# Performance work log

Hardware: AMD Instinct MI355X
Metric: run time of the kernel (lower is better)

## Reference

```python
import jax, jax.numpy as jnp
import numpy as np

N_NODES = 50000
N_EDGES = 800000
H_DIM = 128
N_REL = 40
N_BASES = 4


def setup_inputs() -> dict:
    key = jax.random.key(0)
    ks = jax.random.split(key, 9)
    h = jax.random.normal(ks[0], (N_NODES, H_DIM), jnp.float32)
    norm = jax.random.uniform(ks[1], (N_EDGES, 1), jnp.float32)
    basis_w = jax.random.normal(ks[2], (N_BASES, H_DIM, H_DIM), jnp.float32) * 0.05
    w_comp = jax.random.normal(ks[3], (N_REL, N_BASES), jnp.float32) * 0.5
    loop_w = jax.random.normal(ks[4], (H_DIM, H_DIM), jnp.float32) * 0.05
    bias = jax.random.normal(ks[5], (H_DIM,), jnp.float32) * 0.05
    src = jax.random.randint(ks[6], (N_EDGES,), 0, N_NODES, jnp.int32)
    dst = jax.random.randint(ks[7], (N_EDGES,), 0, N_NODES, jnp.int32)
    etype = jax.random.randint(ks[8], (N_EDGES,), 0, N_REL, jnp.int32)
    return {"h": h, "norm": norm, "basis_w": basis_w, "w_comp": w_comp,
            "loop_w": loop_w, "bias": bias, "src": src, "dst": dst, "etype": etype}


def reference(h, norm, basis_w, w_comp, loop_w, bias, src, dst, etype):
    # RelGraphConv with 'basis' regularizer, one layer (num_hidden_layers=1):
    #   W_r = sum_b w_comp[r, b] * basis_w[b]
    #   m_e = (h[src_e] @ W_{etype_e}) * norm_e
    #   agg[v] = sum_{e: dst_e = v} m_e
    #   out = relu(agg + bias + h @ loop_w)   (dropout = 0)
    # Contraction reordered for memory efficiency: scatter-add per-basis
    # scaled source features first (node-level), then apply small basis GEMMs.
    n = h.shape[0]
    n_bases = basis_w.shape[0]
    coeff = w_comp[etype] * norm          # [E, B] per-edge basis coefficients * norm
    h_src = h[src]                        # [E, D] edge-gathered source features
    agg = jnp.zeros((n, basis_w.shape[2]), dtype=h.dtype)
    for b in range(n_bases):              # small fixed loop over bases
        s_b = jax.ops.segment_sum(coeff[:, b:b + 1] * h_src, dst, num_segments=n)  # [N, D]
        agg = agg + s_b @ basis_w[b]
    return jax.nn.relu(agg + bias + h @ loop_w)
```

## Files before the change

### kernel.cpp

```cpp
#include <hip/hip_runtime.h>
#include <stdint.h>

#define N_NODES 50000
#define N_EDGES 800000
#define H_DIM 128
#define N_REL 40
#define N_BASES 4
#define N_RANGES 196
#define EP_BLOCKS 200
#define EDGES_PER_BLK 4000
#define STAGE_CAP 5120

typedef __attribute__((ext_vector_type(8))) short bf16x8;
typedef __attribute__((ext_vector_type(4))) float f32x4;

__device__ __forceinline__ unsigned short f2bf(float f) {
    unsigned int u = __float_as_uint(f);
    unsigned int r = u + 0x7fffu + ((u >> 16) & 1u);
    return (unsigned short)(r >> 16);
}

__global__ __launch_bounds__(256) void prep_kernel(
        const float* __restrict__ h,
        const float* __restrict__ basis_w, const float* __restrict__ loop_w,
        const int* __restrict__ src, const int* __restrict__ dst,
        const int* __restrict__ etype, const float* __restrict__ norm,
        unsigned short* __restrict__ A, unsigned short* __restrict__ wt3,
        uint2* __restrict__ pkd, int* __restrict__ gcnt) {
    int bid = blockIdx.x;
    if (bid < 3125) {
        int t = bid * 256 + threadIdx.x;
        int row = t >> 4;
        int cb = (t & 15) * 8;
        const float* p = h + (size_t)row * 128 + cb;
        float4 a0 = ((const float4*)p)[0];
        float4 a1 = ((const float4*)p)[1];
        bf16x8 o;
        o[0] = (short)f2bf(a0.x); o[1] = (short)f2bf(a0.y);
        o[2] = (short)f2bf(a0.z); o[3] = (short)f2bf(a0.w);
        o[4] = (short)f2bf(a1.x); o[5] = (short)f2bf(a1.y);
        o[6] = (short)f2bf(a1.z); o[7] = (short)f2bf(a1.w);
        *(bf16x8*)(A + (size_t)row * H_DIM + cb) = o;
    } else if (bid < 3130) {
        int mat = bid - 3125;
        const float* srcm = (mat < 4) ? (basis_w + mat * 16384) : loop_w;
        int koff = (mat < 4) ? (128 + mat * 128) : 0;
        int t = threadIdx.x;
#pragma unroll
        for (int i = 0; i < 16; ++i) {
            int f = t + i * 256;
            int k = f >> 5;
            int j4 = (f & 31) * 4;
            float4 v = ((const float4*)srcm)[f];
            int kg = koff + k;
            int ks = kg >> 5;
            int quad = (kg >> 3) & 3;
            int jj = kg & 7;
            float vv[4] = {v.x, v.y, v.z, v.w};
#pragma unroll
            for (int d = 0; d < 4; ++d) {
                int j = j4 + d;
                int cg = j >> 4;
                int n16 = j & 15;
                wt3[(size_t)((ks * 8 + cg) * 64 + quad * 16 + n16) * 8 + jj] =
                    f2bf(vv[d]);
            }
        }
    } else {
        __shared__ int lhist[N_RANGES];
        int blk = bid - 3130;
        int t = threadIdx.x;
        if (t < N_RANGES) lhist[t] = 0;
        __syncthreads();
        int e0 = blk * EDGES_PER_BLK;
        for (int i = t; i < EDGES_PER_BLK; i += 256) {
            int e = e0 + i;
            int d = dst[e];
            unsigned int nbf = f2bf(norm[e]);
            pkd[e] = make_uint2((unsigned)src[e] | ((unsigned)etype[e] << 20),
                                (unsigned)d | (nbf << 17));
            atomicAdd(&lhist[d >> 8], 1);
        }
        __syncthreads();
        if (t < N_RANGES) gcnt[t * EP_BLOCKS + blk] = lhist[t];
    }
}

__global__ __launch_bounds__(256) void bucket_scan_a(
        const int* __restrict__ gcnt, int* __restrict__ blkbase,
        int* __restrict__ btot) {
    __shared__ int wsum[4];
    int r = blockIdx.x;
    int t = threadIdx.x, lane = t & 63, w = t >> 6;
    int x = (t < EP_BLOCKS) ? gcnt[r * EP_BLOCKS + t] : 0;
    int v = x;
#pragma unroll
    for (int d = 1; d < 64; d <<= 1) {
        int y = __shfl_up(v, d);
        if (lane >= d) v += y;
    }
    if (lane == 63) wsum[w] = v;
    __syncthreads();
    int wpre = 0;
    if (w > 0) wpre += wsum[0];
    if (w > 1) wpre += wsum[1];
    if (w > 2) wpre += wsum[2];
    if (t < EP_BLOCKS) blkbase[r * EP_BLOCKS + t] = wpre + v - x;
    if (t == 255) btot[r] = wpre + v;
}

__global__ __launch_bounds__(256) void binscatter(
        const uint2* __restrict__ pkd, const int* __restrict__ blkbase,
        const int* __restrict__ btot, uint2* __restrict__ bucketed) {
    __shared__ int lcur[N_RANGES];
    __shared__ int wsum[4];
    int t = threadIdx.x, lane = t & 63, w = t >> 6;
    int x = (t < N_RANGES) ? btot[t] : 0;
    int v = x;
#pragma unroll
    for (int d = 1; d < 64; d <<= 1) {
        int y = __shfl_up(v, d);
        if (lane >= d) v += y;
    }
    if (lane == 63) wsum[w] = v;
    __syncthreads();
    int wpre = 0;
    if (w > 0) wpre += wsum[0];
    if (w > 1) wpre += wsum[1];
    if (w > 2) wpre += wsum[2];
    if (t < N_RANGES)
        lcur[t] = (wpre + v - x) + blkbase[t * EP_BLOCKS + blockIdx.x];
    __syncthreads();
    int e0 = blockIdx.x * EDGES_PER_BLK;
    for (int i = t; i < EDGES_PER_BLK; i += 256) {
        uint2 p = pkd[e0 + i];
        int r = (p.y & 0x1FFFF) >> 8;
        int pos = atomicAdd(&lcur[r], 1);
        bucketed[pos] = p;
    }
}

__global__ __launch_bounds__(256) void bucket_sort(
        const int* __restrict__ btot, const uint2* __restrict__ bucketed,
        uint2* __restrict__ sorted_pe, int* __restrict__ offs) {
    __shared__ int hist[256];
    __shared__ int cur[256];
    __shared__ int wsum[4];
    __shared__ int sbeg;
    __shared__ uint2 stage[STAGE_CAP];
    int r = blockIdx.x;
    int t = threadIdx.x, lane = t & 63, w = t >> 6;
    int x = (t < N_RANGES) ? btot[t] : 0;
    int v = x;
#pragma unroll
    for (int d = 1; d < 64; d <<= 1) {
        int y = __shfl_up(v, d);
        if (lane >= d) v += y;
    }
    if (lane == 63) wsum[w] = v;
    hist[t] = 0;
    __syncthreads();
    int wpre = 0;
    if (w > 0) wpre += wsum[0];
    if (w > 1) wpre += wsum[1];
    if (w > 2) wpre += wsum[2];
    if (t == r) sbeg = wpre + v - x;
    __syncthreads();
    int begin = sbeg;
    int end = begin + btot[r];
    int n = end - begin;
    for (int i = begin + t; i < end; i += 256)
        atomicAdd(&hist[bucketed[i].y & 255], 1);
    __syncthreads();
    int x2 = hist[t];
    int v2 = x2;
#pragma unroll
    for (int d = 1; d < 64; d <<= 1) {
        int y = __shfl_up(v2, d);
        if (lane >= d) v2 += y;
    }
    if (lane == 63) wsum[w] = v2;
    __syncthreads();
    int wpre2 = 0;
    if (w > 0) wpre2 += wsum[0];
    if (w > 1) wpre2 += wsum[1];
    if (w > 2) wpre2 += wsum[2];
    int excl_rel = wpre2 + v2 - x2;
    int node = r * 256 + t;
    if (node < N_NODES) offs[node] = begin + excl_rel;
    if (r == N_RANGES - 1 && t == 0) offs[N_NODES] = N_EDGES;
    cur[t] = excl_rel;
    __syncthreads();
    if (n <= STAGE_CAP) {
        for (int i = begin + t; i < end; i += 256) {
            uint2 p = bucketed[i];
            int pos = atomicAdd(&cur[p.y & 255], 1);
            stage[pos] = make_uint2(p.x, (p.y >> 17) << 16);
        }
        __syncthreads();
        for (int i = t; i < n; i += 256)
            sorted_pe[begin + i] = stage[i];
    } else {
        for (int i = begin + t; i < end; i += 256) {
            uint2 p = bucketed[i];
            int pos = atomicAdd(&cur[p.y & 255], 1);
            sorted_pe[begin + pos] = make_uint2(p.x, (p.y >> 17) << 16);
        }
    }
}

__global__ __launch_bounds__(256) void agg_gemm(
        const int* __restrict__ offs, const uint2* __restrict__ sorted_pe,
        const float* __restrict__ w_comp,
        const unsigned short* __restrict__ Ab,
        const unsigned short* __restrict__ wt3,
        const float* __restrict__ bias, float* __restrict__ out) {
    __shared__ __align__(16) unsigned short S[32 * 640];
    int wv = threadIdx.x >> 6;
    int lane = threadIdx.x & 63;
    int nbase = blockIdx.x * 32;
    const unsigned int* Au = (const unsigned int*)Ab;

    for (int q = 0; q < 8; ++q) {
        int row = (wv << 3) + q;
        int v = __builtin_amdgcn_readfirstlane(nbase + row);
        float a0l = 0.f, a0h = 0.f, a1l = 0.f, a1h = 0.f;
        float a2l = 0.f, a2h = 0.f, a3l = 0.f, a3h = 0.f;
        unsigned int hb = 0u;
        if (v < N_NODES) {
            hb = Au[(size_t)v * 64 + lane];
            int begin = offs[v];
            int end = offs[v + 1];
            int j = begin;
            for (; j + 8 <= end; j += 8) {
                uint2 p[8];
                unsigned int u[8];
#pragma unroll
                for (int k = 0; k < 8; ++k) p[k] = sorted_pe[j + k];
#pragma unroll
                for (int k = 0; k < 8; ++k)
                    u[k] = Au[(size_t)(p[k].x & 0xFFFFF) * 64 + lane];
#pragma unroll
                for (int k = 0; k < 8; ++k) {
                    float4 wc = ((const float4*)w_comp)[p[k].x >> 20];
                    float nm = __uint_as_float(p[k].y);
                    float lo = __uint_as_float(u[k] << 16);
                    float hi = __uint_as_float(u[k] & 0xffff0000u);
                    a0l += (wc.x * nm) * lo; a0h += (wc.x * nm) * hi;
                    a1l += (wc.y * nm) * lo; a1h += (wc.y * nm) * hi;
                    a2l += (wc.z * nm) * lo; a2h += (wc.z * nm) * hi;
                    a3l += (wc.w * nm) * lo; a3h += (wc.w * nm) * hi;
                }
            }
            for (; j < end; ++j) {
                uint2 p = sorted_pe[j];
                float4 wc = ((const float4*)w_comp)[p.x >> 20];
                float nm = __uint_as_float(p.y);
                unsigned int u = Au[(size_t)(p.x & 0xFFFFF) * 64 + lane];
                float lo = __uint_as_float(u << 16);
                float hi = __uint_as_float(u & 0xffff0000u);
                a0l += (wc.x * nm) * lo; a0h += (wc.x * nm) * hi;
                a1l += (wc.y * nm) * lo; a1h += (wc.y * nm) * hi;
                a2l += (wc.z * nm) * lo; a2h += (wc.z * nm) * hi;
                a3l += (wc.w * nm) * lo; a3h += (wc.w * nm) * hi;
            }
        }
        char* rp = (char*)S + row * 1280;
        int swz = (row & 7) << 4;
        *(unsigned int*)(rp + ((lane * 4) ^ swz)) = hb;
        *(unsigned int*)(rp + ((256 + lane * 4) ^ swz)) =
            (unsigned int)f2bf(a0l) | ((unsigned int)f2bf(a0h) << 16);
        *(unsigned int*)(rp + ((512 + lane * 4) ^ swz)) =
            (unsigned int)f2bf(a1l) | ((unsigned int)f2bf(a1h) << 16);
        *(unsigned int*)(rp + ((768 + lane * 4) ^ swz)) =
            (unsigned int)f2bf(a2l) | ((unsigned int)f2bf(a2h) << 16);
        *(unsigned int*)(rp + ((1024 + lane * 4) ^ swz)) =
            (unsigned int)f2bf(a3l) | ((unsigned int)f2bf(a3h) << 16);
    }
    __syncthreads();

    int n16 = lane & 15;
    int quad = lane >> 4;
    f32x4 acc[2][2];
#pragma unroll
    for (int rt = 0; rt < 2; ++rt)
#pragma unroll
        for (int c = 0; c < 2; ++c) acc[rt][c] = (f32x4)0.f;

    const char* a0p = (const char*)S + n16 * 1280;
    const char* a1p = (const char*)S + (16 + n16) * 1280;
    int swz2 = (n16 & 7) << 4;
    const unsigned short* bp = wt3 + (size_t)(wv * 2) * 512 + lane * 8;

#pragma unroll
    for (int ks = 0; ks < 20; ++ks) {
        int off = (ks * 64 + quad * 16) ^ swz2;
        bf16x8 a0 = *(const bf16x8*)(a0p + off);
        bf16x8 a1 = *(const bf16x8*)(a1p + off);
        bf16x8 b0 = *(const bf16x8*)(bp + (size_t)ks * 4096);
        bf16x8 b1 = *(const bf16x8*)(bp + (size_t)ks * 4096 + 512);
        acc[0][0] = __builtin_amdgcn_mfma_f32_16x16x32_bf16(a0, b0, acc[0][0], 0, 0, 0);
        acc[1][0] = __builtin_amdgcn_mfma_f32_16x16x32_bf16(a1, b0, acc[1][0], 0, 0, 0);
        acc[0][1] = __builtin_amdgcn_mfma_f32_16x16x32_bf16(a0, b1, acc[0][1], 0, 0, 0);
        acc[1][1] = __builtin_amdgcn_mfma_f32_16x16x32_bf16(a1, b1, acc[1][1], 0, 0, 0);
    }

#pragma unroll
    for (int rt = 0; rt < 2; ++rt) {
#pragma unroll
        for (int c = 0; c < 2; ++c) {
            int col = (wv * 2 + c) * 16 + n16;
            float bv = bias[col];
#pragma unroll
            for (int rg = 0; rg < 4; ++rg) {
                int r = nbase + rt * 16 + quad * 4 + rg;
                if (r < N_NODES)
                    out[(size_t)r * H_DIM + col] = fmaxf(acc[rt][c][rg] + bv, 0.f);
            }
        }
    }
}

extern "C" void kernel_launch(void* const* d_in, const int* in_sizes, int n_in,
                              void* d_out, int out_size, void* d_ws, size_t ws_size,
                              hipStream_t stream) {
    const float* h       = (const float*)d_in[0];
    const float* norm    = (const float*)d_in[1];
    const float* basis_w = (const float*)d_in[2];
    const float* w_comp  = (const float*)d_in[3];
    const float* loop_w  = (const float*)d_in[4];
    const float* bias    = (const float*)d_in[5];
    const int*   src     = (const int*)d_in[6];
    const int*   dst     = (const int*)d_in[7];
    const int*   etype   = (const int*)d_in[8];
    float* out = (float*)d_out;

    char* base = (char*)d_ws;
    unsigned short* wt3       = (unsigned short*)(base + 0);
    unsigned short* A         = (unsigned short*)(base + 163840);
    int*            offs      = (int*)(base + 12963840);
    uint2*          pkd       = (uint2*)(base + 13163848);
    uint2*          bucketed  = (uint2*)(base + 19563848);
    uint2*          sorted_pe = (uint2*)(base + 25963848);
    int*            gcnt      = (int*)(base + 32363848);
    int*            blkbase   = (int*)(base + 32520648);
    int*            btot      = (int*)(base + 32677448);

    prep_kernel<<<3330, 256, 0, stream>>>(h, basis_w, loop_w,
                                          src, dst, etype, norm,
                                          A, wt3, pkd, gcnt);
    bucket_scan_a<<<N_RANGES, 256, 0, stream>>>(gcnt, blkbase, btot);
    binscatter<<<EP_BLOCKS, 256, 0, stream>>>(pkd, blkbase, btot, bucketed);
    bucket_sort<<<N_RANGES, 256, 0, stream>>>(btot, bucketed, sorted_pe, offs);
    agg_gemm<<<1563, 256, 0, stream>>>(offs, sorted_pe, w_comp, A, wt3, bias, out);
}
```

Measured before the change: 193.3 us.

## Precompute per-edge basis coefficients in sort, split agg_gemm over 8 waves

The bucket sort now writes a separate source-index array and a float4 of w_comp[etype]*norm per edge, so the aggregation loop no longer gathers w_comp or multiplies by norm per edge. The aggregation kernel moves to 512 threads (8 waves, 4 rows each, one 16-column MFMA tile per wave). It also replaces the scalar tail loop with a masked 8-wide loop reading padded zero entries. The cost is more sorted-edge traffic (20 bytes per edge instead of 8), traded for less per-edge ALU work and more parallelism per block.

```diff
diff --git a/kernel.cpp b/kernel.cpp
--- a/kernel.cpp
+++ b/kernel.cpp
@@ -88,10 +88,15 @@
 
 __global__ __launch_bounds__(256) void bucket_scan_a(
         const int* __restrict__ gcnt, int* __restrict__ blkbase,
-        int* __restrict__ btot) {
+        int* __restrict__ btot, unsigned* __restrict__ sorted_src,
+        float4* __restrict__ sorted_cf) {
     __shared__ int wsum[4];
     int r = blockIdx.x;
     int t = threadIdx.x, lane = t & 63, w = t >> 6;
+    if (r == 0 && t < 16) {
+        sorted_src[N_EDGES + t] = 0u;
+        sorted_cf[N_EDGES + t] = make_float4(0.f, 0.f, 0.f, 0.f);
+    }
     int x = (t < EP_BLOCKS) ? gcnt[r * EP_BLOCKS + t] : 0;
     int v = x;
 #pragma unroll
@@ -142,7 +147,9 @@
 
 __global__ __launch_bounds__(256) void bucket_sort(
         const int* __restrict__ btot, const uint2* __restrict__ bucketed,
-        uint2* __restrict__ sorted_pe, int* __restrict__ offs) {
+        const float* __restrict__ w_comp,
+        unsigned* __restrict__ sorted_src, float4* __restrict__ sorted_cf,
+        int* __restrict__ offs) {
     __shared__ int hist[256];
     __shared__ int cur[256];
     __shared__ int wsum[4];
@@ -198,20 +205,30 @@
             stage[pos] = make_uint2(p.x, (p.y >> 17) << 16);
         }
         __syncthreads();
-        for (int i = t; i < n; i += 256)
-            sorted_pe[begin + i] = stage[i];
+        for (int i = t; i < n; i += 256) {
+            uint2 p = stage[i];
+            float nm = __uint_as_float(p.y);
+            float4 wc = ((const float4*)w_comp)[p.x >> 20];
+            sorted_src[begin + i] = p.x & 0xFFFFF;
+            sorted_cf[begin + i] =
+                make_float4(wc.x * nm, wc.y * nm, wc.z * nm, wc.w * nm);
+        }
     } else {
         for (int i = begin + t; i < end; i += 256) {
             uint2 p = bucketed[i];
             int pos = atomicAdd(&cur[p.y & 255], 1);
-            sorted_pe[begin + pos] = make_uint2(p.x, (p.y >> 17) << 16);
-        }
-    }
-}
-
-__global__ __launch_bounds__(256) void agg_gemm(
-        const int* __restrict__ offs, const uint2* __restrict__ sorted_pe,
-        const float* __restrict__ w_comp,
+            float nm = __uint_as_float((p.y >> 17) << 16);
+            float4 wc = ((const float4*)w_comp)[p.x >> 20];
+            sorted_src[begin + pos] = p.x & 0xFFFFF;
+            sorted_cf[begin + pos] =
+                make_float4(wc.x * nm, wc.y * nm, wc.z * nm, wc.w * nm);
+        }
+    }
+}
+
+__global__ __launch_bounds__(512, 8) void agg_gemm(
+        const int* __restrict__ offs, const unsigned* __restrict__ ssrc,
+        const float4* __restrict__ scf,
         const unsigned short* __restrict__ Ab,
         const unsigned short* __restrict__ wt3,
         const float* __restrict__ bias, float* __restrict__ out) {
@@ -221,48 +238,46 @@
     int nbase = blockIdx.x * 32;
     const unsigned int* Au = (const unsigned int*)Ab;
 
-    for (int q = 0; q < 8; ++q) {
-        int row = (wv << 3) + q;
+#pragma unroll
+    for (int q = 0; q < 4; ++q) {
+        int row = (wv << 2) + q;
         int v = __builtin_amdgcn_readfirstlane(nbase + row);
         float a0l = 0.f, a0h = 0.f, a1l = 0.f, a1h = 0.f;
         float a2l = 0.f, a2h = 0.f, a3l = 0.f, a3h = 0.f;
         unsigned int hb = 0u;
         if (v < N_NODES) {
             hb = Au[(size_t)v * 64 + lane];
-            int begin = offs[v];
-            int end = offs[v + 1];
-            int j = begin;
-            for (; j + 8 <= end; j += 8) {
-                uint2 p[8];
-                unsigned int u[8];
-#pragma unroll
-                for (int k = 0; k < 8; ++k) p[k] = sorted_pe[j + k];
+            int begin = __builtin_amdgcn_readfirstlane(offs[v]);
+            int end   = __builtin_amdgcn_readfirstlane(offs[v + 1]);
+            for (int j = begin; j < end; j += 8) {
+                int rem = end - j;
+                unsigned su[8];
+                float4 c[8];
+#pragma unroll
+                for (int k = 0; k < 8; ++k) su[k] = ssrc[j + k];
+#pragma unroll
+                for (int k = 0; k < 8; ++k) c[k] = scf[j + k];
+                if (rem < 8) {
+#pragma unroll
+                    for (int k = 0; k < 8; ++k)
+                        if (k >= rem) {
+                            su[k] = 0u;
+                            c[k] = make_float4(0.f, 0.f, 0.f, 0.f);
+                        }
+                }
+                unsigned u[8];
 #pragma unroll
                 for (int k = 0; k < 8; ++k)
-                    u[k] = Au[(size_t)(p[k].x & 0xFFFFF) * 64 + lane];
+                    u[k] = Au[(size_t)su[k] * 64 + lane];
 #pragma unroll
                 for (int k = 0; k < 8; ++k) {
-                    float4 wc = ((const float4*)w_comp)[p[k].x >> 20];
-                    float nm = __uint_as_float(p[k].y);
                     float lo = __uint_as_float(u[k] << 16);
                     float hi = __uint_as_float(u[k] & 0xffff0000u);
-                    a0l += (wc.x * nm) * lo; a0h += (wc.x * nm) * hi;
-                    a1l += (wc.y * nm) * lo; a1h += (wc.y * nm) * hi;
-                    a2l += (wc.z * nm) * lo; a2h += (wc.z * nm) * hi;
-                    a3l += (wc.w * nm) * lo; a3h += (wc.w * nm) * hi;
+                    a0l += c[k].x * lo; a0h += c[k].x * hi;
+                    a1l += c[k].y * lo; a1h += c[k].y * hi;
+                    a2l += c[k].z * lo; a2h += c[k].z * hi;
+                    a3l += c[k].w * lo; a3h += c[k].w * hi;
                 }
-            }
-            for (; j < end; ++j) {
-                uint2 p = sorted_pe[j];
-                float4 wc = ((const float4*)w_comp)[p.x >> 20];
-                float nm = __uint_as_float(p.y);
-                unsigned int u = Au[(size_t)(p.x & 0xFFFFF) * 64 + lane];
-                float lo = __uint_as_float(u << 16);
-                float hi = __uint_as_float(u & 0xffff0000u);
-                a0l += (wc.x * nm) * lo; a0h += (wc.x * nm) * hi;
-                a1l += (wc.y * nm) * lo; a1h += (wc.y * nm) * hi;
-                a2l += (wc.z * nm) * lo; a2h += (wc.z * nm) * hi;
-                a3l += (wc.w * nm) * lo; a3h += (wc.w * nm) * hi;
             }
         }
         char* rp = (char*)S + row * 1280;
@@ -281,43 +296,33 @@
 
     int n16 = lane & 15;
     int quad = lane >> 4;
-    f32x4 acc[2][2];
-#pragma unroll
-    for (int rt = 0; rt < 2; ++rt)
-#pragma unroll
-        for (int c = 0; c < 2; ++c) acc[rt][c] = (f32x4)0.f;
-
-    const char* a0p = (const char*)S + n16 * 1280;
-    const char* a1p = (const char*)S + (16 + n16) * 1280;
+    f32x4 acc0 = (f32x4)0.f, acc1 = (f32x4)0.f;
+
+    const char* s0p = (const char*)S + n16 * 1280;
+    const char* s1p = s0p + 16 * 1280;
     int swz2 = (n16 & 7) << 4;
-    const unsigned short* bp = wt3 + (size_t)(wv * 2) * 512 + lane * 8;
+    const unsigned short* bwp = wt3 + (size_t)wv * 512 + (size_t)lane * 8;
 
 #pragma unroll
     for (int ks = 0; ks < 20; ++ks) {
         int off = (ks * 64 + quad * 16) ^ swz2;
-        bf16x8 a0 = *(const bf16x8*)(a0p + off);
-        bf16x8 a1 = *(const bf16x8*)(a1p + off);
-        bf16x8 b0 = *(const bf16x8*)(bp + (size_t)ks * 4096);
-        bf16x8 b1 = *(const bf16x8*)(bp + (size_t)ks * 4096 + 512);
-        acc[0][0] = __builtin_amdgcn_mfma_f32_16x16x32_bf16(a0, b0, acc[0][0], 0, 0, 0);
-        acc[1][0] = __builtin_amdgcn_mfma_f32_16x16x32_bf16(a1, b0, acc[1][0], 0, 0, 0);
-        acc[0][1] = __builtin_amdgcn_mfma_f32_16x16x32_bf16(a0, b1, acc[0][1], 0, 0, 0);
-        acc[1][1] = __builtin_amdgcn_mfma_f32_16x16x32_bf16(a1, b1, acc[1][1], 0, 0, 0);
-    }
-
-#pragma unroll
-    for (int rt = 0; rt < 2; ++rt) {
-#pragma unroll
-        for (int c = 0; c < 2; ++c) {
-            int col = (wv * 2 + c) * 16 + n16;
-            float bv = bias[col];
-#pragma unroll
-            for (int rg = 0; rg < 4; ++rg) {
-                int r = nbase + rt * 16 + quad * 4 + rg;
-                if (r < N_NODES)
-                    out[(size_t)r * H_DIM + col] = fmaxf(acc[rt][c][rg] + bv, 0.f);
-            }
-        }
+        bf16x8 a0 = *(const bf16x8*)(s0p + off);
+        bf16x8 a1 = *(const bf16x8*)(s1p + off);
+        bf16x8 b  = *(const bf16x8*)(bwp + (size_t)ks * 4096);
+        acc0 = __builtin_amdgcn_mfma_f32_16x16x32_bf16(a0, b, acc0, 0, 0, 0);
+        acc1 = __builtin_amdgcn_mfma_f32_16x16x32_bf16(a1, b, acc1, 0, 0, 0);
+    }
+
+    int col = (wv << 4) + n16;
+    float bv = bias[col];
+#pragma unroll
+    for (int rg = 0; rg < 4; ++rg) {
+        int r0 = nbase + quad * 4 + rg;
+        if (r0 < N_NODES)
+            out[(size_t)r0 * H_DIM + col] = fmaxf(acc0[rg] + bv, 0.f);
+        int r1 = nbase + 16 + quad * 4 + rg;
+        if (r1 < N_NODES)
+            out[(size_t)r1 * H_DIM + col] = fmaxf(acc1[rg] + bv, 0.f);
     }
 }
 
@@ -341,16 +346,20 @@
     int*            offs      = (int*)(base + 12963840);
     uint2*          pkd       = (uint2*)(base + 13163848);
     uint2*          bucketed  = (uint2*)(base + 19563848);
-    uint2*          sorted_pe = (uint2*)(base + 25963848);
-    int*            gcnt      = (int*)(base + 32363848);
-    int*            blkbase   = (int*)(base + 32520648);
-    int*            btot      = (int*)(base + 32677448);
+    float4*         sorted_cf = (float4*)(base + 25963856);
+    unsigned*       sorted_src= (unsigned*)(base + 38764112);
+    int*            gcnt      = (int*)(base + 41964176);
+    int*            blkbase   = (int*)(base + 42120976);
+    int*            btot      = (int*)(base + 42277776);
 
     prep_kernel<<<3330, 256, 0, stream>>>(h, basis_w, loop_w,
                                           src, dst, etype, norm,
                                           A, wt3, pkd, gcnt);
-    bucket_scan_a<<<N_RANGES, 256, 0, stream>>>(gcnt, blkbase, btot);
+    bucket_scan_a<<<N_RANGES, 256, 0, stream>>>(gcnt, blkbase, btot,
+                                                sorted_src, sorted_cf);
     binscatter<<<EP_BLOCKS, 256, 0, stream>>>(pkd, blkbase, btot, bucketed);
-    bucket_sort<<<N_RANGES, 256, 0, stream>>>(btot, bucketed, sorted_pe, offs);
-    agg_gemm<<<1563, 256, 0, stream>>>(offs, sorted_pe, w_comp, A, wt3, bias, out);
-}
+    bucket_sort<<<N_RANGES, 256, 0, stream>>>(btot, bucketed, w_comp,
+                                              sorted_src, sorted_cf, offs);
+    agg_gemm<<<1563, 512, 0, stream>>>(offs, sorted_src, sorted_cf,
+                                       A, wt3, bias, out);
+}
```

Result: faster. 172.4 us (-10.8%).
